# Optimization experiments

Measured on AMD Instinct MI355X. Metric: run time of the kernel, lower is better.

The kernel has to match this reference:

```python
import math
import jax, jax.numpy as jnp
import numpy as np

B, S, D, H, REL_V = 2, 2048, 1024, 16, 64
HD = D // H
EPS = 1e-5


def _layernorm(x, w, b):
    # torch-style: std with Bessel correction (unbiased), divide by (std + eps)
    u = x.mean(-1, keepdims=True)
    xc = x - u
    s = jnp.sqrt((xc * xc).sum(-1, keepdims=True) / (x.shape[-1] - 1))
    return w * (xc / (s + EPS)) + b


def _gelu(x):
    return 0.5 * x * (1 + jnp.tanh(math.sqrt(2 / math.pi) * (x + 0.044715 * x ** 3)))


def setup_inputs() -> dict:
    key = jax.random.key(0)
    ks = jax.random.split(key, 6)
    wscale = 0.02
    return {
        "x": jax.random.normal(ks[0], (B, S, D), jnp.float32),
        "rel": jax.random.randint(ks[1], (B, S, S), 0, REL_V, jnp.int32),
        "ln1_w": jnp.ones((D,), jnp.float32),
        "ln1_b": jnp.zeros((D,), jnp.float32),
        "Wqkv": jax.random.normal(ks[2], (D, 3 * D), jnp.float32) * wscale,
        "bqkv": jnp.zeros((3 * D,), jnp.float32),
        "Wo": jax.random.normal(ks[3], (D, D), jnp.float32) * wscale,
        "bo": jnp.zeros((D,), jnp.float32),
        "rel_emb": jax.random.normal(ks[4], (REL_V, H), jnp.float32) * wscale,
        "ln2_w": jnp.ones((D,), jnp.float32),
        "ln2_b": jnp.zeros((D,), jnp.float32),
        "Wfc": jax.random.normal(ks[5], (D, 4 * D), jnp.float32) * wscale,
        "bfc": jnp.zeros((4 * D,), jnp.float32),
        "Wp": jax.random.normal(jax.random.fold_in(key, 7), (4 * D, D), jnp.float32) * wscale,
        "bp": jnp.zeros((D,), jnp.float32),
    }


def reference(x, rel, ln1_w, ln1_b, Wqkv, bqkv, Wo, bo, rel_emb,
              ln2_w, ln2_b, Wfc, bfc, Wp, bp):
    h = _layernorm(x, ln1_w, ln1_b)
    qkv = h @ Wqkv + bqkv  # [B,S,3D]
    q, k, v = jnp.split(qkv, 3, axis=-1)
    q = q.reshape(B, S, H, HD).transpose(0, 2, 1, 3)  # [B,H,S,HD]
    k = k.reshape(B, S, H, HD).transpose(0, 2, 1, 3)
    v = v.reshape(B, S, H, HD).transpose(0, 2, 1, 3)

    w = jnp.einsum('bhqd,bhkd->bhqk', q, k) / math.sqrt(HD)  # scale=True
    mask = jnp.tril(jnp.ones((S, S), w.dtype))  # causal tril buffer
    w = w * mask - 1e10 * (1 - mask)
    # faithful to original: rel bias multiplies masked logits (zeroing masked -1e10)
    relw = rel_emb[rel]                    # [B,S,S,H]
    relw = relw.transpose(0, 3, 1, 2)      # [B,H,S,S]
    w = w * (relw * mask)
    p = jax.nn.softmax(w, axis=-1)
    a = jnp.einsum('bhqk,bhkd->bhqd', p, v)       # [B,H,S,HD]
    a = a.transpose(0, 2, 1, 3).reshape(B, S, D)  # merge heads
    a = a @ Wo + bo

    x = x + a
    m = _gelu(_layernorm(x, ln2_w, ln2_b) @ Wfc + bfc) @ Wp + bp
    return x + m
```

## Files before the change

### kernel.cpp

```cpp
#include <hip/hip_runtime.h>
#include <hip/hip_bf16.h>
#include <math.h>

using bf16 = __hip_bfloat16;
typedef __bf16 bf16x8 __attribute__((ext_vector_type(8)));
typedef float f32x4 __attribute__((ext_vector_type(4)));

#define SEQ 2048
#define DIM 1024
#define NH 16
#define HDIM 64
#define BATCH 2

__device__ __forceinline__ void load_lds16(const bf16* g, bf16* l) {
  __builtin_amdgcn_global_load_lds((__attribute__((address_space(1))) void*)g,
                                   (__attribute__((address_space(3))) void*)l, 16, 0, 0);
}

__global__ __launch_bounds__(256) void transpose_k(const float* __restrict__ in,
                                                   bf16* __restrict__ out, int R, int C) {
  __shared__ float tile[32][33];
  int c0 = blockIdx.x * 32, r0 = blockIdx.y * 32;
  int tx = threadIdx.x, ty = threadIdx.y;
#pragma unroll
  for (int j = 0; j < 4; ++j)
    tile[ty + 8 * j][tx] = in[(size_t)(r0 + ty + 8 * j) * C + c0 + tx];
  __syncthreads();
#pragma unroll
  for (int j = 0; j < 4; ++j)
    out[(size_t)(c0 + ty + 8 * j) * R + r0 + tx] = __float2bfloat16(tile[tx][ty + 8 * j]);
}

__global__ __launch_bounds__(256) void ln_k(const float* __restrict__ x,
                                            const float* __restrict__ w,
                                            const float* __restrict__ bb,
                                            bf16* __restrict__ out) {
  int row = blockIdx.x, tid = threadIdx.x;
  int wid = tid >> 6, lane = tid & 63;
  const float* xr = x + (size_t)row * DIM;
  float v[4];
#pragma unroll
  for (int j = 0; j < 4; ++j) v[j] = xr[tid + 256 * j];
  float s = v[0] + v[1] + v[2] + v[3];
#pragma unroll
  for (int m = 1; m < 64; m <<= 1) s += __shfl_xor(s, m, 64);
  __shared__ float red[8];
  if (lane == 0) red[wid] = s;
  __syncthreads();
  float mean = (red[0] + red[1] + red[2] + red[3]) * (1.f / DIM);
  float q = 0.f;
#pragma unroll
  for (int j = 0; j < 4; ++j) {
    v[j] -= mean;
    q += v[j] * v[j];
  }
#pragma unroll
  for (int m = 1; m < 64; m <<= 1) q += __shfl_xor(q, m, 64);
  if (lane == 0) red[4 + wid] = q;
  __syncthreads();
  float ssq = red[4] + red[5] + red[6] + red[7];
  float sd = sqrtf(ssq / (float)(DIM - 1));
  float inv = 1.f / (sd + 1e-5f);
#pragma unroll
  for (int j = 0; j < 4; ++j) {
    int c = tid + 256 * j;
    float y = w[c] * (v[j] * inv) + bb[c];
    out[(size_t)row * DIM + c] = __float2bfloat16(y);
  }
}

template <int TM>
__global__ __launch_bounds__(256) void gemm_k(
    const bf16* __restrict__ A, const bf16* __restrict__ Bt, const float* __restrict__ bias,
    int M, int N, int K, int mode,
    bf16* __restrict__ o0, bf16* __restrict__ o1, bf16* __restrict__ o2,
    const float* __restrict__ residf, float* __restrict__ x2out, const float* __restrict__ x2in,
    float* __restrict__ outf) {
  constexpr int MT = TM / 32;
  constexpr int ACH = TM / 8;
  __shared__ bf16 As[TM * 64];
  __shared__ bf16 Bs[128 * 64];
  int tid = threadIdx.x;
  int wid = tid >> 6, lane = tid & 63, quad = lane >> 4, l15 = lane & 15;
  int wm = wid >> 1, wn = wid & 1;
  int m0 = blockIdx.y * TM, n0 = blockIdx.x * 128;
  int rsub = lane >> 3;
  int c8 = (lane & 7) ^ rsub;
  f32x4 acc[MT][4] = {};

  for (int k0 = 0; k0 < K; k0 += 64) {
    __syncthreads();
#pragma unroll
    for (int it = 0; it < ACH / 4; ++it) {
      int c = wid * (ACH / 4) + it;
      int row = c * 8 + rsub;
      load_lds16(A + (size_t)(m0 + row) * K + k0 + c8 * 8, &As[c * 512]);
    }
#pragma unroll
    for (int it = 0; it < 4; ++it) {
      int c = wid * 4 + it;
      int row = c * 8 + rsub;
      load_lds16(Bt + (size_t)(n0 + row) * K + k0 + c8 * 8, &Bs[c * 512]);
    }
    __syncthreads();
#pragma unroll
    for (int ks = 0; ks < 2; ++ks) {
      bf16x8 af[MT], bfr[4];
#pragma unroll
      for (int mt = 0; mt < MT; ++mt) {
        int r = wm * (MT * 16) + mt * 16 + l15;
        af[mt] = *(const bf16x8*)&As[r * 64 + ((ks * 4 + quad) ^ (r & 7)) * 8];
      }
#pragma unroll
      for (int nt = 0; nt < 4; ++nt) {
        int r = wn * 64 + nt * 16 + l15;
        bfr[nt] = *(const bf16x8*)&Bs[r * 64 + ((ks * 4 + quad) ^ (r & 7)) * 8];
      }
#pragma unroll
      for (int mt = 0; mt < MT; ++mt)
#pragma unroll
        for (int nt = 0; nt < 4; ++nt)
          acc[mt][nt] =
              __builtin_amdgcn_mfma_f32_16x16x32_bf16(af[mt], bfr[nt], acc[mt][nt], 0, 0, 0);
    }
  }

#pragma unroll
  for (int mt = 0; mt < MT; ++mt) {
#pragma unroll
    for (int nt = 0; nt < 4; ++nt) {
      int col = n0 + wn * 64 + nt * 16 + l15;
      float bv = bias[col];
      int row_base = m0 + wm * (MT * 16) + mt * 16 + quad * 4;
      if (mode == 0) {
        int which = col >> 10, d = col & 1023, hh = d >> 6, dd = d & 63;
        int b = row_base >> 11, s2 = row_base & 2047;
        if (which == 2) {
          unsigned short pk[4];
#pragma unroll
          for (int r = 0; r < 4; ++r)
            pk[r] = __bfloat16_as_ushort(__float2bfloat16(acc[mt][nt][r] + bv));
          *(uint2*)&o2[(((size_t)b * NH + hh) * HDIM + dd) * SEQ + s2] = *(uint2*)pk;
        } else {
          bf16* dst = which == 0 ? o0 : o1;
#pragma unroll
          for (int r = 0; r < 4; ++r)
            dst[(((size_t)b * NH + hh) * SEQ + s2 + r) * HDIM + dd] =
                __float2bfloat16(acc[mt][nt][r] + bv);
        }
      } else {
#pragma unroll
        for (int r = 0; r < 4; ++r) {
          int row = row_base + r;
          float val = acc[mt][nt][r] + bv;
          if (mode == 1) {
            size_t i = (size_t)row * N + col;
            x2out[i] = residf[i] + val;
          } else if (mode == 2) {
            float t = val;
            float u = 0.7978845608028654f * (t + 0.044715f * t * t * t);
            float g = t / (1.f + __expf(-2.f * u));
            o0[(size_t)row * N + col] = __float2bfloat16(g);
          } else {
            size_t i = (size_t)row * N + col;
            outf[i] = x2in[i] + val;
          }
        }
      }
    }
  }
}

__global__ __launch_bounds__(256) void sufv_k(const bf16* __restrict__ vt,
                                              float* __restrict__ suf) {
  int row = blockIdx.x;
  const bf16* src = vt + (size_t)row * SEQ;
  float* dst = suf + (size_t)row * SEQ;
  int tid = threadIdx.x;
  float v[8];
  float s = 0.f;
#pragma unroll
  for (int j = 0; j < 8; ++j) {
    v[j] = __bfloat162float(src[tid * 8 + j]);
    s += v[j];
  }
  __shared__ float sc[256];
  sc[tid] = s;
  __syncthreads();
  for (int off = 1; off < 256; off <<= 1) {
    float add = (tid + off < 256) ? sc[tid + off] : 0.f;
    __syncthreads();
    sc[tid] += add;
    __syncthreads();
  }
  float run = (tid < 255) ? sc[tid + 1] : 0.f;
#pragma unroll
  for (int j = 7; j >= 0; --j) {
    dst[tid * 8 + j] = run;
    run += v[j];
  }
}

__global__ __launch_bounds__(256) void attn_k(const bf16* __restrict__ q,
                                              const bf16* __restrict__ k,
                                              const bf16* __restrict__ v,
                                              const int* __restrict__ rel,
                                              const float* __restrict__ rel_emb,
                                              const float* __restrict__ suf,
                                              bf16* __restrict__ out) {
  int h = blockIdx.x;
  int qt = (SEQ / 64 - 1) - blockIdx.y;
  int b = blockIdx.z;
  int tid = threadIdx.x;
  int wid = tid >> 6, lane = tid & 63, quad = lane >> 4, l15 = lane & 15;

  __shared__ __align__(16) char SM[50176];
  bf16* Qs = (bf16*)SM;
  bf16* Kb = (bf16*)(SM + 8192);
  bf16* Vb = (bf16*)(SM + 8192 + 16384);
  bf16(*Ps)[72] = (bf16(*)[72])(SM + 40960);
  float(*SufLds)[68] = (float(*)[68])(SM + 8192);

  const size_t bh = (size_t)b * NH + h;
  const bf16* qb = q + (bh * SEQ + (size_t)qt * 64) * HDIM;
  const bf16* kb0 = k + bh * SEQ * HDIM;
  const bf16* vt0 = v + bh * (size_t)HDIM * SEQ;

  float rv = 0.125f * rel_emb[lane * NH + h];

  int rsub = lane >> 3;
  int c8 = (lane & 7) ^ rsub;

#pragma unroll
  for (int it = 0; it < 2; ++it) {
    int c = wid * 2 + it;
    int row = c * 8 + rsub;
    load_lds16(qb + (size_t)row * HDIM + c8 * 8, &Qs[c * 512]);
    load_lds16(kb0 + (size_t)row * HDIM + c8 * 8, &Kb[c * 512]);
    load_lds16(vt0 + (size_t)row * SEQ + c8 * 8, &Vb[c * 512]);
  }

  const int* relq = rel + (size_t)b * SEQ * SEQ + (size_t)qt * 64 * SEQ;
  const int* rp[4];
#pragma unroll
  for (int r = 0; r < 4; ++r) rp[r] = relq + (size_t)(wid * 16 + quad * 4 + r) * SEQ;

  int ridx[4][4];
#pragma unroll
  for (int nt = 0; nt < 4; ++nt)
#pragma unroll
    for (int r = 0; r < 4; ++r) ridx[nt][r] = rp[r][nt * 16 + l15];

  __syncthreads();

  bf16x8 aq[2];
#pragma unroll
  for (int ks = 0; ks < 2; ++ks)
    aq[ks] = *(const bf16x8*)&Qs[(wid * 16 + l15) * 64 + ((ks * 4 + quad) ^ (l15 & 7)) * 8];

  const int q_base = qt * 64 + wid * 16 + quad * 4;
  float l_part[4] = {0.f, 0.f, 0.f, 0.f};
  f32x4 o_acc[4] = {};

  for (int kt = 0; kt <= qt; ++kt) {
    int cur = kt & 1;

    int ridx2[4][4];
    if (kt < qt) {
      bf16* Kd = Kb + (cur ^ 1) * 4096;
      bf16* Vd = Vb + (cur ^ 1) * 4096;
#pragma unroll
      for (int it = 0; it < 2; ++it) {
        int c = wid * 2 + it;
        int row = c * 8 + rsub;
        load_lds16(kb0 + (size_t)((kt + 1) * 64 + row) * HDIM + c8 * 8, &Kd[c * 512]);
        load_lds16(vt0 + (size_t)row * SEQ + (kt + 1) * 64 + c8 * 8, &Vd[c * 512]);
      }
#pragma unroll
      for (int nt = 0; nt < 4; ++nt)
#pragma unroll
        for (int r = 0; r < 4; ++r) ridx2[nt][r] = rp[r][(kt + 1) * 64 + nt * 16 + l15];
    }

    const bf16* Ksb = Kb + cur * 4096;
    const bf16* Vtb = Vb + cur * 4096;

    f32x4 sacc[4] = {};
#pragma unroll
    for (int ks = 0; ks < 2; ++ks) {
#pragma unroll
      for (int nt = 0; nt < 4; ++nt) {
        bf16x8 bfr = *(const bf16x8*)&Ksb[(nt * 16 + l15) * 64 + ((ks * 4 + quad) ^ (l15 & 7)) * 8];
        sacc[nt] = __builtin_amdgcn_mfma_f32_16x16x32_bf16(aq[ks], bfr, sacc[nt], 0, 0, 0);
      }
    }

#pragma unroll
    for (int nt = 0; nt < 4; ++nt) {
#pragma unroll
      for (int r = 0; r < 4; ++r) {
        float m = __shfl(rv, ridx[nt][r], 64);
        float p = __expf(sacc[nt][r] * m);
        if (kt == qt) {
          int k_abs = kt * 64 + nt * 16 + l15;
          if (k_abs > q_base + r) p = 0.f;
        }
        l_part[r] += p;
        Ps[wid * 16 + quad * 4 + r][nt * 16 + l15] = __float2bfloat16(p);
      }
    }

#pragma unroll
    for (int ks = 0; ks < 2; ++ks) {
      bf16x8 af = *(const bf16x8*)&Ps[wid * 16 + l15][ks * 32 + quad * 8];
#pragma unroll
      for (int nt = 0; nt < 4; ++nt) {
        bf16x8 bfr = *(const bf16x8*)&Vtb[(nt * 16 + l15) * 64 + ((ks * 4 + quad) ^ (l15 & 7)) * 8];
        o_acc[nt] = __builtin_amdgcn_mfma_f32_16x16x32_bf16(af, bfr, o_acc[nt], 0, 0, 0);
      }
    }

    __syncthreads();

    if (kt < qt) {
#pragma unroll
      for (int nt = 0; nt < 4; ++nt)
#pragma unroll
        for (int r = 0; r < 4; ++r) ridx[nt][r] = ridx2[nt][r];
    }
  }

#pragma unroll
  for (int r = 0; r < 4; ++r)
#pragma unroll
    for (int m = 1; m < 16; m <<= 1) l_part[r] += __shfl_xor(l_part[r], m, 64);

  const float* sufb = suf + bh * (size_t)HDIM * SEQ + (size_t)qt * 64;
#pragma unroll
  for (int p = 0; p < 4; ++p) {
    int idx = p * 256 + tid;
    int d = idx >> 4, qq = idx & 15;
    *(float4*)&SufLds[d][qq * 4] = *(const float4*)(sufb + (size_t)d * SEQ + qq * 4);
  }
  __syncthreads();

#pragma unroll
  for (int nt = 0; nt < 4; ++nt) {
    int d = nt * 16 + l15;
#pragma unroll
    for (int r = 0; r < 4; ++r) {
      int row = q_base + r;
      int cnt = (SEQ - 1) - row;
      float l = l_part[r] + (float)cnt;
      int q_local = wid * 16 + quad * 4 + r;
      float ov = (o_acc[nt][r] + SufLds[d][q_local]) / l;
      out[((size_t)b * SEQ + row) * DIM + h * HDIM + d] = __float2bfloat16(ov);
    }
  }
}

extern "C" void kernel_launch(void* const* d_in, const int* in_sizes, int n_in,
                              void* d_out, int out_size, void* d_ws, size_t ws_size,
                              hipStream_t stream) {
  const float* x = (const float*)d_in[0];
  const int* rel = (const int*)d_in[1];
  const float* ln1w = (const float*)d_in[2];
  const float* ln1b = (const float*)d_in[3];
  const float* Wqkv = (const float*)d_in[4];
  const float* bqkv = (const float*)d_in[5];
  const float* Wo = (const float*)d_in[6];
  const float* bo = (const float*)d_in[7];
  const float* rel_emb = (const float*)d_in[8];
  const float* ln2w = (const float*)d_in[9];
  const float* ln2b = (const float*)d_in[10];
  const float* Wfc = (const float*)d_in[11];
  const float* bfc = (const float*)d_in[12];
  const float* Wp = (const float*)d_in[13];
  const float* bp = (const float*)d_in[14];
  float* outp = (float*)d_out;

  char* ws = (char*)d_ws;
  const size_t MB = 1u << 20;
  bf16* h = (bf16*)(ws + 0);
  bf16* qb = (bf16*)(ws + 8 * MB);
  bf16* kb = (bf16*)(ws + 16 * MB);
  bf16* vb = (bf16*)(ws + 24 * MB);
  float* x2 = (float*)(ws + 32 * MB);
  float* suf = (float*)(ws + 32 * MB);
  bf16* fcb = (bf16*)(ws + 48 * MB);
  bf16* wqkvT = (bf16*)(ws + 48 * MB);
  bf16* woT = (bf16*)(ws + 54 * MB);
  bf16* wfcT = (bf16*)(ws + 16 * MB);
  bf16* wpT = (bf16*)(ws + 24 * MB);

  dim3 tb(32, 8);
  transpose_k<<<dim3(3072 / 32, 1024 / 32), tb, 0, stream>>>(Wqkv, wqkvT, 1024, 3072);
  transpose_k<<<dim3(1024 / 32, 1024 / 32), tb, 0, stream>>>(Wo, woT, 1024, 1024);

  ln_k<<<BATCH * SEQ, 256, 0, stream>>>(x, ln1w, ln1b, h);

  gemm_k<128><<<dim3(3072 / 128, 4096 / 128), 256, 0, stream>>>(
      h, wqkvT, bqkv, BATCH * SEQ, 3072, 1024, 0, qb, kb, vb, nullptr, nullptr, nullptr,
      nullptr);

  sufv_k<<<BATCH * NH * HDIM, 256, 0, stream>>>(vb, suf);

  attn_k<<<dim3(NH, SEQ / 64, BATCH), 256, 0, stream>>>(qb, kb, vb, rel, rel_emb, suf, h);

  gemm_k<64><<<dim3(1024 / 128, 4096 / 64), 256, 0, stream>>>(
      h, woT, bo, BATCH * SEQ, 1024, 1024, 1, nullptr, nullptr, nullptr, x, x2, nullptr,
      nullptr);

  transpose_k<<<dim3(4096 / 32, 1024 / 32), tb, 0, stream>>>(Wfc, wfcT, 1024, 4096);
  transpose_k<<<dim3(1024 / 32, 4096 / 32), tb, 0, stream>>>(Wp, wpT, 4096, 1024);

  ln_k<<<BATCH * SEQ, 256, 0, stream>>>(x2, ln2w, ln2b, qb);

  gemm_k<128><<<dim3(4096 / 128, 4096 / 128), 256, 0, stream>>>(
      qb, wfcT, bfc, BATCH * SEQ, 4096, 1024, 2, fcb, nullptr, nullptr, nullptr, nullptr,
      nullptr, nullptr);

  gemm_k<64><<<dim3(1024 / 128, 4096 / 64), 256, 0, stream>>>(
      fcb, wpT, bp, BATCH * SEQ, 1024, 4096, 3, nullptr, nullptr, nullptr, nullptr, nullptr, x2,
      outp);
}
```

Before: 437.3 us.

## Restructure attention inner loop: peel diagonal tile, swizzle P, shrink LDS

Q fragments now load straight from global into registers instead of going through LDS, which cuts shared memory from 50176 to 40960 bytes and could allow more resident blocks. The diagonal (masked) key tile is peeled out of the main loop, so off-diagonal iterations skip the causal mask check. The P staging buffer moves to an XOR-swizzled layout to reduce LDS bank conflicts. s_setprio hints are wrapped around the MFMA sections, at the cost of duplicated code for the peeled tile.

```diff
diff --git a/kernel.cpp b/kernel.cpp
--- a/kernel.cpp
+++ b/kernel.cpp
@@ -201,6 +201,8 @@
   }
 }
 
+__device__ __forceinline__ int pswz(int row) { return (row & 7) ^ (((row >> 3) & 1) << 1); }
+
 __global__ __launch_bounds__(256) void attn_k(const bf16* __restrict__ q,
                                               const bf16* __restrict__ k,
                                               const bf16* __restrict__ v,
@@ -214,12 +216,11 @@
   int tid = threadIdx.x;
   int wid = tid >> 6, lane = tid & 63, quad = lane >> 4, l15 = lane & 15;
 
-  __shared__ __align__(16) char SM[50176];
-  bf16* Qs = (bf16*)SM;
-  bf16* Kb = (bf16*)(SM + 8192);
-  bf16* Vb = (bf16*)(SM + 8192 + 16384);
-  bf16(*Ps)[72] = (bf16(*)[72])(SM + 40960);
-  float(*SufLds)[68] = (float(*)[68])(SM + 8192);
+  __shared__ __align__(16) char SM[40960];
+  bf16* Kb = (bf16*)SM;
+  bf16* Vb = (bf16*)(SM + 16384);
+  bf16* Ps = (bf16*)(SM + 32768);
+  float(*SufLds)[68] = (float(*)[68])SM;
 
   const size_t bh = (size_t)b * NH + h;
   const bf16* qb = q + (bh * SEQ + (size_t)qt * 64) * HDIM;
@@ -231,11 +232,15 @@
   int rsub = lane >> 3;
   int c8 = (lane & 7) ^ rsub;
 
+  bf16x8 aq[2];
+#pragma unroll
+  for (int ks = 0; ks < 2; ++ks)
+    aq[ks] = *(const bf16x8*)(qb + (size_t)(wid * 16 + l15) * HDIM + ks * 32 + quad * 8);
+
 #pragma unroll
   for (int it = 0; it < 2; ++it) {
     int c = wid * 2 + it;
     int row = c * 8 + rsub;
-    load_lds16(qb + (size_t)row * HDIM + c8 * 8, &Qs[c * 512]);
     load_lds16(kb0 + (size_t)row * HDIM + c8 * 8, &Kb[c * 512]);
     load_lds16(vt0 + (size_t)row * SEQ + c8 * 8, &Vb[c * 512]);
   }
@@ -253,20 +258,18 @@
 
   __syncthreads();
 
-  bf16x8 aq[2];
-#pragma unroll
-  for (int ks = 0; ks < 2; ++ks)
-    aq[ks] = *(const bf16x8*)&Qs[(wid * 16 + l15) * 64 + ((ks * 4 + quad) ^ (l15 & 7)) * 8];
-
   const int q_base = qt * 64 + wid * 16 + quad * 4;
+  const int prow_w = wid * 16 + quad * 4;
+  const int prow_r = wid * 16 + l15;
+  const int psw_r = pswz(prow_r);
   float l_part[4] = {0.f, 0.f, 0.f, 0.f};
   f32x4 o_acc[4] = {};
 
-  for (int kt = 0; kt <= qt; ++kt) {
+  for (int kt = 0; kt < qt; ++kt) {
     int cur = kt & 1;
 
     int ridx2[4][4];
-    if (kt < qt) {
+    {
       bf16* Kd = Kb + (cur ^ 1) * 4096;
       bf16* Vd = Vb + (cur ^ 1) * 4096;
 #pragma unroll
@@ -286,6 +289,7 @@
     const bf16* Vtb = Vb + cur * 4096;
 
     f32x4 sacc[4] = {};
+    __builtin_amdgcn_s_setprio(1);
 #pragma unroll
     for (int ks = 0; ks < 2; ++ks) {
 #pragma unroll
@@ -294,6 +298,7 @@
         sacc[nt] = __builtin_amdgcn_mfma_f32_16x16x32_bf16(aq[ks], bfr, sacc[nt], 0, 0, 0);
       }
     }
+    __builtin_amdgcn_s_setprio(0);
 
 #pragma unroll
     for (int nt = 0; nt < 4; ++nt) {
@@ -301,33 +306,78 @@
       for (int r = 0; r < 4; ++r) {
         float m = __shfl(rv, ridx[nt][r], 64);
         float p = __expf(sacc[nt][r] * m);
-        if (kt == qt) {
-          int k_abs = kt * 64 + nt * 16 + l15;
-          if (k_abs > q_base + r) p = 0.f;
-        }
         l_part[r] += p;
-        Ps[wid * 16 + quad * 4 + r][nt * 16 + l15] = __float2bfloat16(p);
-      }
-    }
-
+        int row = prow_w + r;
+        int sw = (nt * 2 + (l15 >> 3)) ^ pswz(row);
+        Ps[row * 64 + sw * 8 + (l15 & 7)] = __float2bfloat16(p);
+      }
+    }
+
+    __builtin_amdgcn_s_setprio(1);
 #pragma unroll
     for (int ks = 0; ks < 2; ++ks) {
-      bf16x8 af = *(const bf16x8*)&Ps[wid * 16 + l15][ks * 32 + quad * 8];
+      bf16x8 af = *(const bf16x8*)&Ps[prow_r * 64 + ((ks * 4 + quad) ^ psw_r) * 8];
 #pragma unroll
       for (int nt = 0; nt < 4; ++nt) {
         bf16x8 bfr = *(const bf16x8*)&Vtb[(nt * 16 + l15) * 64 + ((ks * 4 + quad) ^ (l15 & 7)) * 8];
         o_acc[nt] = __builtin_amdgcn_mfma_f32_16x16x32_bf16(af, bfr, o_acc[nt], 0, 0, 0);
       }
     }
-
-    __syncthreads();
-
-    if (kt < qt) {
-#pragma unroll
-      for (int nt = 0; nt < 4; ++nt)
-#pragma unroll
-        for (int r = 0; r < 4; ++r) ridx[nt][r] = ridx2[nt][r];
-    }
+    __builtin_amdgcn_s_setprio(0);
+
+    __syncthreads();
+
+#pragma unroll
+    for (int nt = 0; nt < 4; ++nt)
+#pragma unroll
+      for (int r = 0; r < 4; ++r) ridx[nt][r] = ridx2[nt][r];
+  }
+
+  {
+    int cur = qt & 1;
+    const bf16* Ksb = Kb + cur * 4096;
+    const bf16* Vtb = Vb + cur * 4096;
+
+    f32x4 sacc[4] = {};
+    __builtin_amdgcn_s_setprio(1);
+#pragma unroll
+    for (int ks = 0; ks < 2; ++ks) {
+#pragma unroll
+      for (int nt = 0; nt < 4; ++nt) {
+        bf16x8 bfr = *(const bf16x8*)&Ksb[(nt * 16 + l15) * 64 + ((ks * 4 + quad) ^ (l15 & 7)) * 8];
+        sacc[nt] = __builtin_amdgcn_mfma_f32_16x16x32_bf16(aq[ks], bfr, sacc[nt], 0, 0, 0);
+      }
+    }
+    __builtin_amdgcn_s_setprio(0);
+
+#pragma unroll
+    for (int nt = 0; nt < 4; ++nt) {
+#pragma unroll
+      for (int r = 0; r < 4; ++r) {
+        float m = __shfl(rv, ridx[nt][r], 64);
+        float p = __expf(sacc[nt][r] * m);
+        int k_abs = qt * 64 + nt * 16 + l15;
+        if (k_abs > q_base + r) p = 0.f;
+        l_part[r] += p;
+        int row = prow_w + r;
+        int sw = (nt * 2 + (l15 >> 3)) ^ pswz(row);
+        Ps[row * 64 + sw * 8 + (l15 & 7)] = __float2bfloat16(p);
+      }
+    }
+
+    __builtin_amdgcn_s_setprio(1);
+#pragma unroll
+    for (int ks = 0; ks < 2; ++ks) {
+      bf16x8 af = *(const bf16x8*)&Ps[prow_r * 64 + ((ks * 4 + quad) ^ psw_r) * 8];
+#pragma unroll
+      for (int nt = 0; nt < 4; ++nt) {
+        bf16x8 bfr = *(const bf16x8*)&Vtb[(nt * 16 + l15) * 64 + ((ks * 4 + quad) ^ (l15 & 7)) * 8];
+        o_acc[nt] = __builtin_amdgcn_mfma_f32_16x16x32_bf16(af, bfr, o_acc[nt], 0, 0, 0);
+      }
+    }
+    __builtin_amdgcn_s_setprio(0);
+
+    __syncthreads();
   }
 
 #pragma unroll
```

New measurement: 424.0 us. 3.0% less time.
